# Kernel tuning notes

Measured on AMD Instinct MI355X. Metric: run time of the kernel, lower is better.

The kernel has to match this reference:

```python
import jax, jax.numpy as jnp
import numpy as np

X_SCALE, X_ZP = 0.03, -66.0
Y_SCALE, Y_ZP = 0.025, 160.0  # per-tensor quant params for uint8 y


def setup_inputs() -> dict:
    key = jax.random.key(0)
    kx, ky = jax.random.split(key)
    # x simulates int8 values in [-128, 127], stored as fp32
    x = jax.random.randint(kx, (7, 8, 1024, 1024), 0, 256).astype(jnp.float32) - 128.0
    # y simulates uint8 values in [0, 255], stored as fp32
    y = jax.random.randint(ky, (8, 1024, 1024), 0, 256).astype(jnp.float32)
    return {"x": x, "y": y}


def reference(x, y):
    # dequantize: (q - zero_point) * scale
    qx = (x - X_ZP) * X_SCALE              # [7, B, M, K] fp32
    qy = (y - Y_ZP) * Y_SCALE              # [B, K, N] fp32
    # torch.matmul broadcasting: 4D @ 3D -> [7, B, M, N]
    return jnp.einsum('sbmk,bkn->sbmn', qx, qy)
```

## Files before the change

kernel.cpp:

```cpp
#include <hip/hip_runtime.h>
#include <cstdint>


#define NG 56

typedef int v4i  __attribute__((ext_vector_type(4)));
typedef int v16i __attribute__((ext_vector_type(16)));

#define GLOAD16(g, l) __builtin_amdgcn_global_load_lds( \
    (const __attribute__((address_space(1))) void*)(g), \
    (__attribute__((address_space(3))) void*)(l), 16, 0, 0)

__device__ __forceinline__ unsigned pack4(float4 v, float& s) {
    s += (v.x + v.y) + (v.z + v.w);
    unsigned b0 = __float_as_uint(v.x + 8388736.0f);
    unsigned b1 = __float_as_uint(v.y + 8388736.0f);
    unsigned b2 = __float_as_uint(v.z + 8388736.0f);
    unsigned b3 = __float_as_uint(v.w + 8388736.0f);
    return ((b0 & 0xFFu) | ((b1 & 0xFFu) << 8) | ((b2 & 0xFFu) << 16) | ((b3 & 0xFFu) << 24))
           ^ 0x80808080u;
}

__global__ __launch_bounds__(256) void k_prep_x(const float* __restrict__ x,
                                                unsigned char* __restrict__ xb,
                                                float* __restrict__ rx) {
    int row  = blockIdx.x * 4 + (threadIdx.x >> 6);
    int lane = threadIdx.x & 63;
    const float* src = x + (size_t)row * 1024;
    float s = 0.f;
#pragma unroll
    for (int it = 0; it < 4; ++it) {
        float4 v = *(const float4*)(src + it * 256 + lane * 4);
        unsigned p = pack4(v, s);
        *(unsigned*)&xb[(size_t)row * 1024 + it * 256 + lane * 4] = p;
    }
#pragma unroll
    for (int off = 32; off > 0; off >>= 1) s += __shfl_down(s, off);
    if (lane == 0) rx[row] = s;
}

__global__ __launch_bounds__(256) void k_prep_y(const float* __restrict__ y,
                                                unsigned char* __restrict__ yt,
                                                float* __restrict__ cy) {
    __shared__ float tile[64][65];
    __shared__ float csum[4][64];
    int b  = blockIdx.x >> 8;
    int t  = blockIdx.x & 255;
    int kt = (t >> 4) * 64, nt = (t & 15) * 64;
    int tx = threadIdx.x & 63;
    int ty = threadIdx.x >> 6;
    const float* src = y + ((size_t)b << 20) + (size_t)kt * 1024 + nt;
    float part = 0.f;
#pragma unroll
    for (int r = 0; r < 16; ++r) {
        int kk = r * 4 + ty;
        float v = src[(size_t)kk * 1024 + tx];
        tile[kk][tx] = v;
        part += v;
    }
    csum[ty][tx] = part;
    __syncthreads();
    if (threadIdx.x < 64) {
        float s = csum[0][tx] + csum[1][tx] + csum[2][tx] + csum[3][tx];
        atomicAdd(&cy[b * 1024 + nt + tx], s);
    }
    int ky = threadIdx.x & 15;
    int ny = threadIdx.x >> 4;
#pragma unroll
    for (int r = 0; r < 4; ++r) {
        int nn = r * 16 + ny;
        unsigned b0 = __float_as_uint(tile[ky * 4 + 0][nn] + 8388608.0f);
        unsigned b1 = __float_as_uint(tile[ky * 4 + 1][nn] + 8388608.0f);
        unsigned b2 = __float_as_uint(tile[ky * 4 + 2][nn] + 8388608.0f);
        unsigned b3 = __float_as_uint(tile[ky * 4 + 3][nn] + 8388608.0f);
        unsigned p = ((b0 & 0xFFu) | ((b1 & 0xFFu) << 8) | ((b2 & 0xFFu) << 16) |
                      ((b3 & 0xFFu) << 24)) ^ 0x80808080u;
        *(unsigned*)&yt[((size_t)b << 20) + (size_t)(nt + nn) * 1024 + kt + ky * 4] = p;
    }
}

__global__ __launch_bounds__(256) void k_gemm(const unsigned char* __restrict__ xb,
                                              const unsigned char* __restrict__ yt,
                                              const float* __restrict__ rx,
                                              const float* __restrict__ cy,
                                              float* __restrict__ out) {
    __shared__ __align__(16) unsigned char As[2][128 * 64];
    __shared__ __align__(16) unsigned char Bs[2][128 * 64];

    int bid = blockIdx.x;
    int wg  = (bid & 7) * (NG * 64 / 8) + (bid >> 3);
    int g   = wg >> 6;
    int t   = wg & 63;
    int m0  = (t >> 3) * 128, n0 = (t & 7) * 128;
    int b   = g & 7;

    int tid = threadIdx.x, lane = tid & 63, w = tid >> 6;
    int wm = w >> 1, wn = w & 1;

    const unsigned char* Ab = xb + (size_t)g * 1048576 + (size_t)m0 * 1024;
    const unsigned char* Bb = yt + ((size_t)b << 20) + (size_t)n0 * 1024;

    int srow   = tid >> 2;
    int schunk = (tid & 3) ^ (srow & 3);
    size_t off0 = (size_t)srow * 1024 + schunk * 16;
    size_t off1 = off0 + 64 * 1024;
    int dst0 = (tid & ~63) * 16;
    int dst1 = (256 + (tid & ~63)) * 16;

#define STAGE(buf, kt) do {                                   \
    GLOAD16(Ab + off0 + (size_t)(kt) * 64, &As[buf][dst0]);   \
    GLOAD16(Ab + off1 + (size_t)(kt) * 64, &As[buf][dst1]);   \
    GLOAD16(Bb + off0 + (size_t)(kt) * 64, &Bs[buf][dst0]);   \
    GLOAD16(Bb + off1 + (size_t)(kt) * 64, &Bs[buf][dst1]);   \
} while (0)

    v16i acc[2][2];
#pragma unroll
    for (int i = 0; i < 2; ++i)
#pragma unroll
        for (int j = 0; j < 2; ++j)
#pragma unroll
            for (int q = 0; q < 16; ++q) acc[i][j][q] = 0;

    int arow = lane & 31, hi = lane >> 5, rm = lane & 3;
    int rA0 = (wm * 64 + arow) * 64, rA1 = (wm * 64 + 32 + arow) * 64;
    int rB0 = (wn * 64 + arow) * 64, rB1 = (wn * 64 + 32 + arow) * 64;
    int c0 = ((0 + hi) ^ rm) * 16;
    int c1 = ((2 + hi) ^ rm) * 16;

    STAGE(0, 0);
    asm volatile("s_waitcnt vmcnt(0)" ::: "memory");
    __syncthreads();

    int cur = 0;
    for (int kt = 0; kt < 16; ++kt) {
        if (kt < 15) STAGE(cur ^ 1, kt + 1);

        v4i a0k0 = *(const v4i*)&As[cur][rA0 + c0];
        v4i a1k0 = *(const v4i*)&As[cur][rA1 + c0];
        v4i b0k0 = *(const v4i*)&Bs[cur][rB0 + c0];
        v4i b1k0 = *(const v4i*)&Bs[cur][rB1 + c0];
        v4i a0k1 = *(const v4i*)&As[cur][rA0 + c1];
        v4i a1k1 = *(const v4i*)&As[cur][rA1 + c1];
        v4i b0k1 = *(const v4i*)&Bs[cur][rB0 + c1];
        v4i b1k1 = *(const v4i*)&Bs[cur][rB1 + c1];

        acc[0][0] = __builtin_amdgcn_mfma_i32_32x32x32_i8(a0k0, b0k0, acc[0][0], 0, 0, 0);
        acc[0][1] = __builtin_amdgcn_mfma_i32_32x32x32_i8(a0k0, b1k0, acc[0][1], 0, 0, 0);
        acc[1][0] = __builtin_amdgcn_mfma_i32_32x32x32_i8(a1k0, b0k0, acc[1][0], 0, 0, 0);
        acc[1][1] = __builtin_amdgcn_mfma_i32_32x32x32_i8(a1k0, b1k0, acc[1][1], 0, 0, 0);
        acc[0][0] = __builtin_amdgcn_mfma_i32_32x32x32_i8(a0k1, b0k1, acc[0][0], 0, 0, 0);
        acc[0][1] = __builtin_amdgcn_mfma_i32_32x32x32_i8(a0k1, b1k1, acc[0][1], 0, 0, 0);
        acc[1][0] = __builtin_amdgcn_mfma_i32_32x32x32_i8(a1k1, b0k1, acc[1][0], 0, 0, 0);
        acc[1][1] = __builtin_amdgcn_mfma_i32_32x32x32_i8(a1k1, b1k1, acc[1][1], 0, 0, 0);

        if (kt < 15) {
            asm volatile("s_waitcnt vmcnt(0)" ::: "memory");
            __syncthreads();
        }
        cur ^= 1;
    }
#undef STAGE

    const float* rxp = rx + g * 1024 + m0 + wm * 64;
    const float* cyp = cy + b * 1024 + n0 + wn * 64;
    float* og = out + (size_t)g * 1048576 + (size_t)(m0 + wm * 64) * 1024 + n0 + wn * 64;
    int col = lane & 31, r4 = hi * 4;
#pragma unroll
    for (int fi = 0; fi < 2; ++fi)
#pragma unroll
        for (int fj = 0; fj < 2; ++fj) {
            int cc = fj * 32 + col;
            float cv = cyp[cc];
            v16i v = acc[fi][fj];
#pragma unroll
            for (int q = 0; q < 16; ++q) {
                int rl = (q & 3) + 8 * (q >> 2) + r4;
                float rxv = rxp[fi * 32 + rl];
                og[(size_t)(fi * 32 + rl) * 1024 + cc] =
                    7.5e-4f * ((float)v[q] - 32.0f * rxv + 66.0f * cv - 10813440.0f);
            }
        }
}

__global__ void k_naive(const float* __restrict__ x, const float* __restrict__ y,
                        float* __restrict__ out) {
    int g = blockIdx.z, b = g & 7;
    int tx = threadIdx.x, ty = threadIdx.y;
    int m = blockIdx.y * 16 + ty, n = blockIdx.x * 16 + tx;
    __shared__ float a[16][17], bs[16][17];
    float s = 0.f;
    for (int kt = 0; kt < 64; ++kt) {
        a[ty][tx]  = x[(size_t)g * 1048576 + (size_t)m * 1024 + kt * 16 + tx];
        bs[ty][tx] = y[(size_t)b * 1048576 + (size_t)(kt * 16 + ty) * 1024 + n];
        __syncthreads();
#pragma unroll
        for (int j = 0; j < 16; ++j)
            s += ((a[ty][j] + 66.0f) * 0.03f) * ((bs[j][tx] - 160.0f) * 0.025f);
        __syncthreads();
    }
    out[(size_t)g * 1048576 + (size_t)m * 1024 + n] = s;
}

extern "C" void kernel_launch(void* const* d_in, const int* in_sizes, int n_in,
                              void* d_out, int out_size, void* d_ws, size_t ws_size,
                              hipStream_t stream) {
    const float* x = (const float*)d_in[0];
    const float* y = (const float*)d_in[1];
    float* out = (float*)d_out;

    const size_t CY_OFF = 0;
    const size_t RX_OFF = 32768;
    const size_t YT_OFF = 262144;
    const size_t XB_OFF = 262144 + 8388608ull;
    const size_t NEED   = XB_OFF + 58720256ull;

    if (ws_size >= NEED) {
        float* cy         = (float*)((char*)d_ws + CY_OFF);
        float* rx         = (float*)((char*)d_ws + RX_OFF);
        unsigned char* yt = (unsigned char*)((char*)d_ws + YT_OFF);
        unsigned char* xb = (unsigned char*)((char*)d_ws + XB_OFF);
        hipMemsetAsync(cy, 0, 32768, stream);
        k_prep_x<<<14336, 256, 0, stream>>>(x, xb, rx);
        k_prep_y<<<2048, 256, 0, stream>>>(y, yt, cy);
        k_gemm<<<NG * 64, 256, 0, stream>>>(xb, yt, rx, cy, out);
    } else {
        dim3 grid(64, 64, NG), blk(16, 16);
        k_naive<<<grid, blk, 0, stream>>>(x, y, out);
    }
}
```

Before: 210.6 us.

## Deepen GEMM K-loop to a 4-buffer pipeline and change LDS swizzle key

The int8 MFMA GEMM moves from double buffering to four LDS buffers, keeping three K-tiles of global-to-LDS loads in flight. Partial `s_waitcnt vmcnt` counts wait only for the tile about to be used, and the loop ends with three peeled compute steps. The XOR swizzle key now uses bits 1-2 of the row index instead of bits 0-1, with matching read offsets, to spread LDS bank accesses for the 16-byte fragment reads. The cost is that LDS per block doubles to 64 KB, which may lower how many blocks fit on each CU.

```diff
diff --git a/kernel.cpp b/kernel.cpp
--- a/kernel.cpp
+++ b/kernel.cpp
@@ -84,8 +84,8 @@
                                               const float* __restrict__ rx,
                                               const float* __restrict__ cy,
                                               float* __restrict__ out) {
-    __shared__ __align__(16) unsigned char As[2][128 * 64];
-    __shared__ __align__(16) unsigned char Bs[2][128 * 64];
+    __shared__ __align__(16) unsigned char As[4][128 * 64];
+    __shared__ __align__(16) unsigned char Bs[4][128 * 64];
 
     int bid = blockIdx.x;
     int wg  = (bid & 7) * (NG * 64 / 8) + (bid >> 3);
@@ -101,7 +101,7 @@
     const unsigned char* Bb = yt + ((size_t)b << 20) + (size_t)n0 * 1024;
 
     int srow   = tid >> 2;
-    int schunk = (tid & 3) ^ (srow & 3);
+    int schunk = (tid & 3) ^ ((srow >> 1) & 3);
     size_t off0 = (size_t)srow * 1024 + schunk * 16;
     size_t off1 = off0 + 64 * 1024;
     int dst0 = (tid & ~63) * 16;
@@ -122,44 +122,51 @@
 #pragma unroll
             for (int q = 0; q < 16; ++q) acc[i][j][q] = 0;
 
-    int arow = lane & 31, hi = lane >> 5, rm = lane & 3;
-    int rA0 = (wm * 64 + arow) * 64, rA1 = (wm * 64 + 32 + arow) * 64;
-    int rB0 = (wn * 64 + arow) * 64, rB1 = (wn * 64 + 32 + arow) * 64;
-    int c0 = ((0 + hi) ^ rm) * 16;
-    int c1 = ((2 + hi) ^ rm) * 16;
+    int arow = lane & 31, hi = lane >> 5, key = (lane >> 1) & 3;
+    int rA0 = (wm * 64 + arow) * 64, rA1 = rA0 + 32 * 64;
+    int rB0 = (wn * 64 + arow) * 64, rB1 = rB0 + 32 * 64;
+    int c0 = (hi ^ key) * 16;
+    int c1 = ((2 + hi) ^ key) * 16;
+
+#define COMPUTE(bi) do {                                                         \
+    v4i a0k0 = *(const v4i*)&As[bi][rA0 + c0];                                   \
+    v4i a1k0 = *(const v4i*)&As[bi][rA1 + c0];                                   \
+    v4i b0k0 = *(const v4i*)&Bs[bi][rB0 + c0];                                   \
+    v4i b1k0 = *(const v4i*)&Bs[bi][rB1 + c0];                                   \
+    v4i a0k1 = *(const v4i*)&As[bi][rA0 + c1];                                   \
+    v4i a1k1 = *(const v4i*)&As[bi][rA1 + c1];                                   \
+    v4i b0k1 = *(const v4i*)&Bs[bi][rB0 + c1];                                   \
+    v4i b1k1 = *(const v4i*)&Bs[bi][rB1 + c1];                                   \
+    acc[0][0] = __builtin_amdgcn_mfma_i32_32x32x32_i8(a0k0, b0k0, acc[0][0], 0, 0, 0); \
+    acc[0][1] = __builtin_amdgcn_mfma_i32_32x32x32_i8(a0k0, b1k0, acc[0][1], 0, 0, 0); \
+    acc[1][0] = __builtin_amdgcn_mfma_i32_32x32x32_i8(a1k0, b0k0, acc[1][0], 0, 0, 0); \
+    acc[1][1] = __builtin_amdgcn_mfma_i32_32x32x32_i8(a1k0, b1k0, acc[1][1], 0, 0, 0); \
+    acc[0][0] = __builtin_amdgcn_mfma_i32_32x32x32_i8(a0k1, b0k1, acc[0][0], 0, 0, 0); \
+    acc[0][1] = __builtin_amdgcn_mfma_i32_32x32x32_i8(a0k1, b1k1, acc[0][1], 0, 0, 0); \
+    acc[1][0] = __builtin_amdgcn_mfma_i32_32x32x32_i8(a1k1, b0k1, acc[1][0], 0, 0, 0); \
+    acc[1][1] = __builtin_amdgcn_mfma_i32_32x32x32_i8(a1k1, b1k1, acc[1][1], 0, 0, 0); \
+} while (0)
 
     STAGE(0, 0);
+    STAGE(1, 1);
+    STAGE(2, 2);
+
+    for (int kt = 0; kt < 13; ++kt) {
+        asm volatile("s_waitcnt vmcnt(8)" ::: "memory");
+        __syncthreads();
+        STAGE((kt + 3) & 3, kt + 3);
+        COMPUTE(kt & 3);
+    }
+    asm volatile("s_waitcnt vmcnt(8)" ::: "memory");
+    __syncthreads();
+    COMPUTE(1);
+    asm volatile("s_waitcnt vmcnt(4)" ::: "memory");
+    __syncthreads();
+    COMPUTE(2);
     asm volatile("s_waitcnt vmcnt(0)" ::: "memory");
     __syncthreads();
-
-    int cur = 0;
-    for (int kt = 0; kt < 16; ++kt) {
-        if (kt < 15) STAGE(cur ^ 1, kt + 1);
-
-        v4i a0k0 = *(const v4i*)&As[cur][rA0 + c0];
-        v4i a1k0 = *(const v4i*)&As[cur][rA1 + c0];
-        v4i b0k0 = *(const v4i*)&Bs[cur][rB0 + c0];
-        v4i b1k0 = *(const v4i*)&Bs[cur][rB1 + c0];
-        v4i a0k1 = *(const v4i*)&As[cur][rA0 + c1];
-        v4i a1k1 = *(const v4i*)&As[cur][rA1 + c1];
-        v4i b0k1 = *(const v4i*)&Bs[cur][rB0 + c1];
-        v4i b1k1 = *(const v4i*)&Bs[cur][rB1 + c1];
-
-        acc[0][0] = __builtin_amdgcn_mfma_i32_32x32x32_i8(a0k0, b0k0, acc[0][0], 0, 0, 0);
-        acc[0][1] = __builtin_amdgcn_mfma_i32_32x32x32_i8(a0k0, b1k0, acc[0][1], 0, 0, 0);
-        acc[1][0] = __builtin_amdgcn_mfma_i32_32x32x32_i8(a1k0, b0k0, acc[1][0], 0, 0, 0);
-        acc[1][1] = __builtin_amdgcn_mfma_i32_32x32x32_i8(a1k0, b1k0, acc[1][1], 0, 0, 0);
-        acc[0][0] = __builtin_amdgcn_mfma_i32_32x32x32_i8(a0k1, b0k1, acc[0][0], 0, 0, 0);
-        acc[0][1] = __builtin_amdgcn_mfma_i32_32x32x32_i8(a0k1, b1k1, acc[0][1], 0, 0, 0);
-        acc[1][0] = __builtin_amdgcn_mfma_i32_32x32x32_i8(a1k1, b0k1, acc[1][0], 0, 0, 0);
-        acc[1][1] = __builtin_amdgcn_mfma_i32_32x32x32_i8(a1k1, b1k1, acc[1][1], 0, 0, 0);
-
-        if (kt < 15) {
-            asm volatile("s_waitcnt vmcnt(0)" ::: "memory");
-            __syncthreads();
-        }
-        cur ^= 1;
-    }
+    COMPUTE(3);
+#undef COMPUTE
 #undef STAGE
 
     const float* rxp = rx + g * 1024 + m0 + wm * 64;
```

Result: slower. 226.0 us (+7.3%).

## Enlarge GEMM tiles to 256x256 with 4-stage LDS pipeline and 512 threads

Applied to the files above, without the earlier changes.

The int8 MFMA GEMM moves from 128x128 tiles with 256 threads and double buffering to 256x256 tiles with 8 waves and a four-deep LDS ring buffer. Loads run three k-tiles ahead with partial vmcnt waits, split half-stage loads interleaved with compute, and s_setprio raised around the MFMA groups. The aim is to cut global traffic per FLOP and hide load latency better. The cost is 128 KB of LDS per block (one block per CU), more accumulator registers, and only 896 blocks, which may leave the wave tail unbalanced.

```diff
diff --git a/kernel.cpp b/kernel.cpp
--- a/kernel.cpp
+++ b/kernel.cpp
@@ -10,6 +10,8 @@
 #define GLOAD16(g, l) __builtin_amdgcn_global_load_lds( \
     (const __attribute__((address_space(1))) void*)(g), \
     (__attribute__((address_space(3))) void*)(l), 16, 0, 0)
+
+#define MFMA_I8(a, b, c) __builtin_amdgcn_mfma_i32_32x32x32_i8(a, b, c, 0, 0, 0)
 
 __device__ __forceinline__ unsigned pack4(float4 v, float& s) {
     s += (v.x + v.y) + (v.z + v.w);
@@ -79,95 +81,151 @@
     }
 }
 
-__global__ __launch_bounds__(256) void k_gemm(const unsigned char* __restrict__ xb,
+__global__ __launch_bounds__(512) void k_gemm(const unsigned char* __restrict__ xb,
                                               const unsigned char* __restrict__ yt,
                                               const float* __restrict__ rx,
                                               const float* __restrict__ cy,
                                               float* __restrict__ out) {
-    __shared__ __align__(16) unsigned char As[2][128 * 64];
-    __shared__ __align__(16) unsigned char Bs[2][128 * 64];
+    __shared__ __align__(16) unsigned char As[4][256 * 64];
+    __shared__ __align__(16) unsigned char Bs[4][256 * 64];
 
     int bid = blockIdx.x;
-    int wg  = (bid & 7) * (NG * 64 / 8) + (bid >> 3);
-    int g   = wg >> 6;
-    int t   = wg & 63;
-    int m0  = (t >> 3) * 128, n0 = (t & 7) * 128;
+    int wg  = (bid & 7) * 112 + (bid >> 3);
+    int g   = wg >> 4;
+    int t   = wg & 15;
+    int m0  = (t >> 2) * 256, n0 = (t & 3) * 256;
     int b   = g & 7;
 
     int tid = threadIdx.x, lane = tid & 63, w = tid >> 6;
-    int wm = w >> 1, wn = w & 1;
+    int wm = w >> 2, wn = w & 3;
 
     const unsigned char* Ab = xb + (size_t)g * 1048576 + (size_t)m0 * 1024;
     const unsigned char* Bb = yt + ((size_t)b << 20) + (size_t)n0 * 1024;
 
-    int srow   = tid >> 2;
-    int schunk = (tid & 3) ^ (srow & 3);
-    size_t off0 = (size_t)srow * 1024 + schunk * 16;
-    size_t off1 = off0 + 64 * 1024;
+    int cid0 = tid, cid1 = 512 + tid;
+    size_t soff0 = (size_t)(cid0 >> 2) * 1024 + (size_t)(((cid0 & 3) ^ ((cid0 >> 3) & 3)) * 16);
+    size_t soff1 = (size_t)(cid1 >> 2) * 1024 + (size_t)(((cid1 & 3) ^ ((cid1 >> 3) & 3)) * 16);
     int dst0 = (tid & ~63) * 16;
-    int dst1 = (256 + (tid & ~63)) * 16;
-
-#define STAGE(buf, kt) do {                                   \
-    GLOAD16(Ab + off0 + (size_t)(kt) * 64, &As[buf][dst0]);   \
-    GLOAD16(Ab + off1 + (size_t)(kt) * 64, &As[buf][dst1]);   \
-    GLOAD16(Bb + off0 + (size_t)(kt) * 64, &Bs[buf][dst0]);   \
-    GLOAD16(Bb + off1 + (size_t)(kt) * 64, &Bs[buf][dst1]);   \
-} while (0)
-
-    v16i acc[2][2];
-#pragma unroll
-    for (int i = 0; i < 2; ++i)
+    int dst1 = (512 + (tid & ~63)) * 16;
+
+    v16i acc[4][2];
+#pragma unroll
+    for (int i = 0; i < 4; ++i)
 #pragma unroll
         for (int j = 0; j < 2; ++j)
 #pragma unroll
             for (int q = 0; q < 16; ++q) acc[i][j][q] = 0;
 
-    int arow = lane & 31, hi = lane >> 5, rm = lane & 3;
-    int rA0 = (wm * 64 + arow) * 64, rA1 = (wm * 64 + 32 + arow) * 64;
-    int rB0 = (wn * 64 + arow) * 64, rB1 = (wn * 64 + 32 + arow) * 64;
-    int c0 = ((0 + hi) ^ rm) * 16;
-    int c1 = ((2 + hi) ^ rm) * 16;
-
-    STAGE(0, 0);
-    asm volatile("s_waitcnt vmcnt(0)" ::: "memory");
-    __syncthreads();
-
-    int cur = 0;
-    for (int kt = 0; kt < 16; ++kt) {
-        if (kt < 15) STAGE(cur ^ 1, kt + 1);
-
-        v4i a0k0 = *(const v4i*)&As[cur][rA0 + c0];
-        v4i a1k0 = *(const v4i*)&As[cur][rA1 + c0];
-        v4i b0k0 = *(const v4i*)&Bs[cur][rB0 + c0];
-        v4i b1k0 = *(const v4i*)&Bs[cur][rB1 + c0];
-        v4i a0k1 = *(const v4i*)&As[cur][rA0 + c1];
-        v4i a1k1 = *(const v4i*)&As[cur][rA1 + c1];
-        v4i b0k1 = *(const v4i*)&Bs[cur][rB0 + c1];
-        v4i b1k1 = *(const v4i*)&Bs[cur][rB1 + c1];
-
-        acc[0][0] = __builtin_amdgcn_mfma_i32_32x32x32_i8(a0k0, b0k0, acc[0][0], 0, 0, 0);
-        acc[0][1] = __builtin_amdgcn_mfma_i32_32x32x32_i8(a0k0, b1k0, acc[0][1], 0, 0, 0);
-        acc[1][0] = __builtin_amdgcn_mfma_i32_32x32x32_i8(a1k0, b0k0, acc[1][0], 0, 0, 0);
-        acc[1][1] = __builtin_amdgcn_mfma_i32_32x32x32_i8(a1k0, b1k0, acc[1][1], 0, 0, 0);
-        acc[0][0] = __builtin_amdgcn_mfma_i32_32x32x32_i8(a0k1, b0k1, acc[0][0], 0, 0, 0);
-        acc[0][1] = __builtin_amdgcn_mfma_i32_32x32x32_i8(a0k1, b1k1, acc[0][1], 0, 0, 0);
-        acc[1][0] = __builtin_amdgcn_mfma_i32_32x32x32_i8(a1k1, b0k1, acc[1][0], 0, 0, 0);
-        acc[1][1] = __builtin_amdgcn_mfma_i32_32x32x32_i8(a1k1, b1k1, acc[1][1], 0, 0, 0);
-
-        if (kt < 15) {
-            asm volatile("s_waitcnt vmcnt(0)" ::: "memory");
-            __syncthreads();
+    int arow = lane & 31, hi = lane >> 5, key = (lane >> 1) & 3;
+    int rA0 = (wm * 128 +  0 + arow) * 64;
+    int rA1 = (wm * 128 + 32 + arow) * 64;
+    int rA2 = (wm * 128 + 64 + arow) * 64;
+    int rA3 = (wm * 128 + 96 + arow) * 64;
+    int rB0 = (wn * 64 +  0 + arow) * 64;
+    int rB1 = (wn * 64 + 32 + arow) * 64;
+    int ck0 = (hi ^ key) * 16;
+    int ck1 = ((2 + hi) ^ key) * 16;
+
+#define STAGE_J0(buf, kt) do {                                      \
+    GLOAD16(Ab + (size_t)(kt) * 64 + soff0, &As[buf][dst0]);        \
+    GLOAD16(Bb + (size_t)(kt) * 64 + soff0, &Bs[buf][dst0]);        \
+} while (0)
+#define STAGE_J1(buf, kt) do {                                      \
+    GLOAD16(Ab + (size_t)(kt) * 64 + soff1, &As[buf][dst1]);        \
+    GLOAD16(Bb + (size_t)(kt) * 64 + soff1, &Bs[buf][dst1]);        \
+} while (0)
+
+#define BARRIER_FENCE() do {                   \
+    __builtin_amdgcn_s_barrier();              \
+    asm volatile("" ::: "memory");             \
+    __builtin_amdgcn_sched_barrier(0);         \
+} while (0)
+
+#define MFMA8(A0, A1, A2, A3, B0, B1) do {     \
+    __builtin_amdgcn_s_setprio(1);             \
+    acc[0][0] = MFMA_I8(A0, B0, acc[0][0]);    \
+    acc[0][1] = MFMA_I8(A0, B1, acc[0][1]);    \
+    acc[1][0] = MFMA_I8(A1, B0, acc[1][0]);    \
+    acc[1][1] = MFMA_I8(A1, B1, acc[1][1]);    \
+    acc[2][0] = MFMA_I8(A2, B0, acc[2][0]);    \
+    acc[2][1] = MFMA_I8(A2, B1, acc[2][1]);    \
+    acc[3][0] = MFMA_I8(A3, B0, acc[3][0]);    \
+    acc[3][1] = MFMA_I8(A3, B1, acc[3][1]);    \
+    __builtin_amdgcn_s_setprio(0);             \
+} while (0)
+
+    STAGE_J0(0, 0); STAGE_J1(0, 0);
+    STAGE_J0(1, 1); STAGE_J1(1, 1);
+    STAGE_J0(2, 2); STAGE_J1(2, 2);
+
+    for (int kt = 0; kt < 13; ++kt) {
+        int bi = kt & 3, pb = (kt + 3) & 3;
+        asm volatile("s_waitcnt vmcnt(8)" ::: "memory");
+        BARRIER_FENCE();
+        {
+            v4i a0 = *(const v4i*)&As[bi][rA0 + ck0];
+            v4i a1 = *(const v4i*)&As[bi][rA1 + ck0];
+            v4i a2 = *(const v4i*)&As[bi][rA2 + ck0];
+            v4i a3 = *(const v4i*)&As[bi][rA3 + ck0];
+            v4i b0 = *(const v4i*)&Bs[bi][rB0 + ck0];
+            v4i b1 = *(const v4i*)&Bs[bi][rB1 + ck0];
+            STAGE_J0(pb, kt + 3);
+            BARRIER_FENCE();
+            MFMA8(a0, a1, a2, a3, b0, b1);
         }
-        cur ^= 1;
-    }
-#undef STAGE
-
-    const float* rxp = rx + g * 1024 + m0 + wm * 64;
+        {
+            v4i a0 = *(const v4i*)&As[bi][rA0 + ck1];
+            v4i a1 = *(const v4i*)&As[bi][rA1 + ck1];
+            v4i a2 = *(const v4i*)&As[bi][rA2 + ck1];
+            v4i a3 = *(const v4i*)&As[bi][rA3 + ck1];
+            v4i b0 = *(const v4i*)&Bs[bi][rB0 + ck1];
+            v4i b1 = *(const v4i*)&Bs[bi][rB1 + ck1];
+            STAGE_J1(pb, kt + 3);
+            BARRIER_FENCE();
+            MFMA8(a0, a1, a2, a3, b0, b1);
+        }
+    }
+
+#define TAIL_TILE(bi, VM) do {                                       \
+    asm volatile("s_waitcnt vmcnt(" #VM ")" ::: "memory");           \
+    BARRIER_FENCE();                                                 \
+    {                                                                \
+        v4i a0 = *(const v4i*)&As[bi][rA0 + ck0];                    \
+        v4i a1 = *(const v4i*)&As[bi][rA1 + ck0];                    \
+        v4i a2 = *(const v4i*)&As[bi][rA2 + ck0];                    \
+        v4i a3 = *(const v4i*)&As[bi][rA3 + ck0];                    \
+        v4i b0 = *(const v4i*)&Bs[bi][rB0 + ck0];                    \
+        v4i b1 = *(const v4i*)&Bs[bi][rB1 + ck0];                    \
+        BARRIER_FENCE();                                             \
+        MFMA8(a0, a1, a2, a3, b0, b1);                               \
+    }                                                                \
+    {                                                                \
+        v4i a0 = *(const v4i*)&As[bi][rA0 + ck1];                    \
+        v4i a1 = *(const v4i*)&As[bi][rA1 + ck1];                    \
+        v4i a2 = *(const v4i*)&As[bi][rA2 + ck1];                    \
+        v4i a3 = *(const v4i*)&As[bi][rA3 + ck1];                    \
+        v4i b0 = *(const v4i*)&Bs[bi][rB0 + ck1];                    \
+        v4i b1 = *(const v4i*)&Bs[bi][rB1 + ck1];                    \
+        BARRIER_FENCE();                                             \
+        MFMA8(a0, a1, a2, a3, b0, b1);                               \
+    }                                                                \
+} while (0)
+
+    TAIL_TILE(1, 8);
+    TAIL_TILE(2, 4);
+    TAIL_TILE(3, 0);
+#undef TAIL_TILE
+#undef MFMA8
+#undef BARRIER_FENCE
+#undef STAGE_J0
+#undef STAGE_J1
+
+    const float* rxp = rx + g * 1024 + m0 + wm * 128;
     const float* cyp = cy + b * 1024 + n0 + wn * 64;
-    float* og = out + (size_t)g * 1048576 + (size_t)(m0 + wm * 64) * 1024 + n0 + wn * 64;
+    float* og = out + (size_t)g * 1048576 + (size_t)(m0 + wm * 128) * 1024 + n0 + wn * 64;
     int col = lane & 31, r4 = hi * 4;
 #pragma unroll
-    for (int fi = 0; fi < 2; ++fi)
+    for (int fi = 0; fi < 4; ++fi)
 #pragma unroll
         for (int fj = 0; fj < 2; ++fj) {
             int cc = fj * 32 + col;
@@ -223,7 +281,7 @@
         hipMemsetAsync(cy, 0, 32768, stream);
         k_prep_x<<<14336, 256, 0, stream>>>(x, xb, rx);
         k_prep_y<<<2048, 256, 0, stream>>>(y, yt, cy);
-        k_gemm<<<NG * 64, 256, 0, stream>>>(xb, yt, rx, cy, out);
+        k_gemm<<<NG * 16, 512, 0, stream>>>(xb, yt, rx, cy, out);
     } else {
         dim3 grid(64, 64, NG), blk(16, 16);
         k_naive<<<grid, blk, 0, stream>>>(x, y, out);
```

Result: faster. 195.8 us (-7.0%).
